# Optimization experiments

Hardware: AMD Instinct MI355X
Metric: run time of the kernel (lower is better)

## Reference

```python
import jax, jax.numpy as jnp
import numpy as np

P, G, N = 32, 256, 6890  # preds, gallery size, SMPL vertices per person


def _procrustes_v2v(pred, gt):
    """Similarity (Procrustes) align pred->gt, return mean per-vertex L2 error.
    pred, gt: (M, 3) point clouds (M = 2*N, both people jointly aligned)."""
    mu_p = pred.mean(axis=0)
    mu_g = gt.mean(axis=0)
    Xp = pred - mu_p
    Xg = gt - mu_g
    var_p = jnp.sum(Xp * Xp)
    K = Xp.T @ Xg                      # (3,3) cross-covariance
    U, s, Vh = jnp.linalg.svd(K)
    V = Vh.T
    d = jnp.sign(jnp.linalg.det(V @ U.T))  # reflection fix
    D = jnp.stack([jnp.ones_like(d), jnp.ones_like(d), d])
    R = (V * D[None, :]) @ U.T         # rotation, det(R)=+1
    scale = jnp.sum(s * D) / var_p
    aligned = scale * (Xp @ R.T) + mu_g
    return jnp.linalg.norm(aligned - gt, axis=-1).mean()


def setup_inputs() -> dict:
    key = jax.random.key(0)
    k1, k2 = jax.random.split(key)
    pred_vertices = jax.random.normal(k1, (P, 2, N, 3), dtype=jnp.float32)
    target = jax.random.normal(k2, (G, 2, N, 3), dtype=jnp.float32)
    return {"pred_vertices": pred_vertices, "target": target}


def reference(pred_vertices, target):
    # flatten the two-person meshes into a single joint point cloud per sample
    pred = pred_vertices.reshape(pred_vertices.shape[0], -1, 3)  # (P, 2N, 3)
    gt = target.reshape(target.shape[0], -1, 3)                  # (G, 2N, 3)
    # all-pairs procrustes v2v errors: (P, G)
    pair_err = jax.vmap(lambda p: jax.vmap(lambda g: _procrustes_v2v(p, g))(gt))(pred)
    mapping = jnp.argmin(pair_err, axis=1)   # best gt index per prediction
    min_error = jnp.min(pair_err, axis=1)    # its v2v error
    return mapping, min_error
```

## Files before the change

### kernel.cpp

```cpp
#include <hip/hip_runtime.h>
#include <math.h>

#define P_ 32
#define G_ 256
#define NV 6890
#define M_ (2 * NV)
#define QUADS (M_ / 4)
#define NPAIR (P_ * G_)

struct WS {
    float mu_p[P_][3];
    float var_p[P_];
    float mu_g[G_][3];
    float At[NPAIR][12];
    float Kmat[NPAIR][9];
    float pair_err[NPAIR];
};

__device__ inline double block_reduce(double v, double* smem) {
#pragma unroll
    for (int off = 32; off > 0; off >>= 1) v += __shfl_down(v, off, 64);
    int wid  = threadIdx.x >> 6;
    int lane = threadIdx.x & 63;
    __syncthreads();
    if (lane == 0) smem[wid] = v;
    __syncthreads();
    double r = 0.0;
    if (threadIdx.x == 0) {
        int nw = blockDim.x >> 6;
        for (int w = 0; w < nw; ++w) r += smem[w];
    }
    return r;
}

__global__ __launch_bounds__(256) void stats_all(const float* __restrict__ pred,
                                                 const float* __restrict__ gt, WS* ws) {
    int b = blockIdx.x;
    bool isP = (b < P_);
    const float* base = isP ? pred + (size_t)b * (M_ * 3)
                            : gt + (size_t)(b - P_) * (M_ * 3);
    double sx = 0, sy = 0, sz = 0, sq = 0;
    for (int q = threadIdx.x; q < QUADS; q += 256) {
        const float4* p4 = (const float4*)(base + 12 * (size_t)q);
        float4 a = p4[0], c = p4[1], d = p4[2];
        sx += (double)a.x + (double)a.w + (double)c.z + (double)d.y;
        sy += (double)a.y + (double)c.x + (double)c.w + (double)d.z;
        sz += (double)a.z + (double)c.y + (double)d.x + (double)d.w;
        if (isP) {
            sq += (double)a.x * a.x + (double)a.y * a.y + (double)a.z * a.z +
                  (double)a.w * a.w + (double)c.x * c.x + (double)c.y * c.y +
                  (double)c.z * c.z + (double)c.w * c.w + (double)d.x * d.x +
                  (double)d.y * d.y + (double)d.z * d.z + (double)d.w * d.w;
        }
    }
    __shared__ double smem[4];
    double rx = block_reduce(sx, smem);
    double ry = block_reduce(sy, smem);
    double rz = block_reduce(sz, smem);
    double rq = block_reduce(sq, smem);
    if (threadIdx.x == 0) {
        double mx = rx / M_, my = ry / M_, mz = rz / M_;
        if (isP) {
            ws->mu_p[b][0] = (float)mx;
            ws->mu_p[b][1] = (float)my;
            ws->mu_p[b][2] = (float)mz;
            ws->var_p[b] = (float)(rq - (mx * mx + my * my + mz * mz) * (double)M_);
        } else {
            ws->mu_g[b - P_][0] = (float)mx;
            ws->mu_g[b - P_][1] = (float)my;
            ws->mu_g[b - P_][2] = (float)mz;
        }
    }
}

#define LOAD_QUAD(BASE, Q, X, Y, Z)                                     \
    {                                                                   \
        const float4* _p4 = (const float4*)((BASE) + 12 * (size_t)(Q)); \
        float4 _a = _p4[0], _c = _p4[1], _d = _p4[2];                   \
        X[0] = _a.x; X[1] = _a.w; X[2] = _c.z; X[3] = _d.y;             \
        Y[0] = _a.y; Y[1] = _c.x; Y[2] = _c.w; Y[3] = _d.z;             \
        Z[0] = _a.z; Z[1] = _c.y; Z[2] = _d.x; Z[3] = _d.w;             \
    }

__global__ __launch_bounds__(256, 2) void crosscov_r(const float* __restrict__ pred,
                                                     const float* __restrict__ gt,
                                                     WS* __restrict__ ws) {
    int bx = blockIdx.x;
    int gbase = (bx & 63) * 4;
    int pbase = (bx >> 6) * 4;
    int t = threadIdx.x;

    const float* pb[4];
    const float* gb[4];
#pragma unroll
    for (int j = 0; j < 4; ++j) {
        pb[j] = pred + (size_t)(pbase + j) * (M_ * 3);
        gb[j] = gt + (size_t)(gbase + j) * (M_ * 3);
    }

    float acc[16][9];
#pragma unroll
    for (int q = 0; q < 16; ++q)
#pragma unroll
        for (int j = 0; j < 9; ++j) acc[q][j] = 0.f;

    for (int q = t; q < QUADS; q += 256) {
        float px[4][4], py[4][4], pz[4][4];
#pragma unroll
        for (int j = 0; j < 4; ++j) LOAD_QUAD(pb[j], q, px[j], py[j], pz[j]);
#pragma unroll
        for (int gg = 0; gg < 4; ++gg) {
            float gx[4], gy[4], gz[4];
            LOAD_QUAD(gb[gg], q, gx, gy, gz);
#pragma unroll
            for (int pp = 0; pp < 4; ++pp) {
                float* a = acc[gg * 4 + pp];
#pragma unroll
                for (int k = 0; k < 4; ++k) {
                    a[0] = fmaf(px[pp][k], gx[k], a[0]);
                    a[1] = fmaf(px[pp][k], gy[k], a[1]);
                    a[2] = fmaf(px[pp][k], gz[k], a[2]);
                    a[3] = fmaf(py[pp][k], gx[k], a[3]);
                    a[4] = fmaf(py[pp][k], gy[k], a[4]);
                    a[5] = fmaf(py[pp][k], gz[k], a[5]);
                    a[6] = fmaf(pz[pp][k], gx[k], a[6]);
                    a[7] = fmaf(pz[pp][k], gy[k], a[7]);
                    a[8] = fmaf(pz[pp][k], gz[k], a[8]);
                }
            }
        }
    }

#pragma unroll
    for (int q = 0; q < 16; ++q)
#pragma unroll
        for (int j = 0; j < 9; ++j) {
            float v = acc[q][j];
            v += __shfl_xor(v, 1);  v += __shfl_xor(v, 2);
            v += __shfl_xor(v, 4);  v += __shfl_xor(v, 8);
            v += __shfl_xor(v, 16); v += __shfl_xor(v, 32);
            acc[q][j] = v;
        }
    __shared__ float part[4][144];
    int lane = t & 63, wave = t >> 6;
    if (lane == 0) {
#pragma unroll
        for (int q = 0; q < 16; ++q)
#pragma unroll
            for (int j = 0; j < 9; ++j) part[wave][q * 9 + j] = acc[q][j];
    }
    __syncthreads();
    if (t < 144) {
        float s = part[0][t] + part[1][t] + part[2][t] + part[3][t];
        int idx = t / 9, j = t % 9;
        int gg = idx >> 2, pp = idx & 3;
        ws->Kmat[(gbase + gg) * P_ + (pbase + pp)][j] = s;
    }
}

__global__ __launch_bounds__(256) void pair_svd(WS* ws) {
    int pair = blockIdx.x * blockDim.x + threadIdx.x;
    if (pair >= NPAIR) return;
    int p = pair & 31;
    int g = pair >> 5;

    double K[3][3];
#pragma unroll
    for (int a = 0; a < 3; ++a)
#pragma unroll
        for (int b = 0; b < 3; ++b) K[a][b] = (double)ws->Kmat[pair][3 * a + b];
    {
        double mp[3] = { ws->mu_p[p][0], ws->mu_p[p][1], ws->mu_p[p][2] };
        double mg[3] = { ws->mu_g[g][0], ws->mu_g[g][1], ws->mu_g[g][2] };
#pragma unroll
        for (int a = 0; a < 3; ++a)
#pragma unroll
            for (int b = 0; b < 3; ++b)
                K[a][b] -= (double)M_ * mp[a] * mg[b];
    }

    double S[3][3];
#pragma unroll
    for (int a = 0; a < 3; ++a)
#pragma unroll
        for (int b = 0; b < 3; ++b) {
            double acc = 0.0;
#pragma unroll
            for (int c = 0; c < 3; ++c) acc += K[c][a] * K[c][b];
            S[a][b] = acc;
        }

    double V[3][3] = { {1, 0, 0}, {0, 1, 0}, {0, 0, 1} };
    double tr = S[0][0] + S[1][1] + S[2][2];
    double tol = 1e-30 * tr * tr + 1e-300;
    const int PP[3] = {0, 0, 1};
    const int QQ[3] = {1, 2, 2};
    for (int sweep = 0; sweep < 30; ++sweep) {
        double off = S[0][1] * S[0][1] + S[0][2] * S[0][2] + S[1][2] * S[1][2];
        if (off <= tol) break;
        for (int r3 = 0; r3 < 3; ++r3) {
            int pq = PP[r3], qq = QQ[r3];
            double apq = S[pq][qq];
            if (apq == 0.0) continue;
            double theta = (S[qq][qq] - S[pq][pq]) / (2.0 * apq);
            double tt = copysign(1.0, theta) / (fabs(theta) + sqrt(theta * theta + 1.0));
            double c = 1.0 / sqrt(tt * tt + 1.0);
            double sj = tt * c;
            for (int r = 0; r < 3; ++r) {
                double srp = S[r][pq], srq = S[r][qq];
                S[r][pq] = c * srp - sj * srq;
                S[r][qq] = sj * srp + c * srq;
            }
            for (int cc = 0; cc < 3; ++cc) {
                double spr = S[pq][cc], sqr = S[qq][cc];
                S[pq][cc] = c * spr - sj * sqr;
                S[qq][cc] = sj * spr + c * sqr;
            }
            for (int r = 0; r < 3; ++r) {
                double vrp = V[r][pq], vrq = V[r][qq];
                V[r][pq] = c * vrp - sj * vrq;
                V[r][qq] = sj * vrp + c * vrq;
            }
        }
    }

    double lam[3] = { S[0][0], S[1][1], S[2][2] };
    int idx[3] = { 0, 1, 2 };
    if (lam[idx[0]] < lam[idx[1]]) { int tt = idx[0]; idx[0] = idx[1]; idx[1] = tt; }
    if (lam[idx[0]] < lam[idx[2]]) { int tt = idx[0]; idx[0] = idx[2]; idx[2] = tt; }
    if (lam[idx[1]] < lam[idx[2]]) { int tt = idx[1]; idx[1] = idx[2]; idx[2] = tt; }
    double Vs[3][3];
    double sv[3];
#pragma unroll
    for (int i = 0; i < 3; ++i) {
        double l = lam[idx[i]];
        sv[i] = sqrt(l > 0.0 ? l : 0.0);
        for (int r = 0; r < 3; ++r) Vs[r][i] = V[r][idx[i]];
    }

    double U[3][3];
#pragma unroll
    for (int i = 0; i < 3; ++i) {
        double kx = K[0][0] * Vs[0][i] + K[0][1] * Vs[1][i] + K[0][2] * Vs[2][i];
        double ky = K[1][0] * Vs[0][i] + K[1][1] * Vs[1][i] + K[1][2] * Vs[2][i];
        double kz = K[2][0] * Vs[0][i] + K[2][1] * Vs[1][i] + K[2][2] * Vs[2][i];
        double inv = (sv[i] > 1e-12 * sv[0] && sv[i] > 0.0) ? 1.0 / sv[i] : 0.0;
        U[0][i] = kx * inv; U[1][i] = ky * inv; U[2][i] = kz * inv;
    }
    if (sv[2] <= 1e-12 * sv[0] || sv[0] == 0.0) {
        U[0][2] = U[1][0] * U[2][1] - U[2][0] * U[1][1];
        U[1][2] = U[2][0] * U[0][1] - U[0][0] * U[2][1];
        U[2][2] = U[0][0] * U[1][1] - U[1][0] * U[0][1];
    }

    double detK = K[0][0] * (K[1][1] * K[2][2] - K[1][2] * K[2][1])
                - K[0][1] * (K[1][0] * K[2][2] - K[1][2] * K[2][0])
                + K[0][2] * (K[1][0] * K[2][1] - K[1][1] * K[2][0]);
    double d = (detK >= 0.0) ? 1.0 : -1.0;

    double varp = (double)ws->var_p[p];
    double scale = (sv[0] + sv[1] + d * sv[2]) / varp;

    float A[9];
#pragma unroll
    for (int a = 0; a < 3; ++a)
#pragma unroll
        for (int b = 0; b < 3; ++b) {
            double r = Vs[a][0] * U[b][0] + Vs[a][1] * U[b][1] + d * Vs[a][2] * U[b][2];
            A[3 * a + b] = (float)(scale * r);
        }
    double mp[3] = { ws->mu_p[p][0], ws->mu_p[p][1], ws->mu_p[p][2] };
    double mg[3] = { ws->mu_g[g][0], ws->mu_g[g][1], ws->mu_g[g][2] };
    float tvec[3];
#pragma unroll
    for (int a = 0; a < 3; ++a)
        tvec[a] = (float)(mg[a] - ((double)A[3 * a + 0] * mp[0] + (double)A[3 * a + 1] * mp[1] +
                                   (double)A[3 * a + 2] * mp[2]));

#pragma unroll
    for (int j = 0; j < 9; ++j) ws->At[pair][j] = A[j];
#pragma unroll
    for (int j = 0; j < 3; ++j) ws->At[pair][9 + j] = tvec[j];
}

__global__ __launch_bounds__(256, 3) void pair_error_r(const float* __restrict__ pred,
                                                       const float* __restrict__ gt,
                                                       WS* __restrict__ ws) {
    int bx = blockIdx.x;
    int gbase = (bx & 63) * 4;
    int pbase = (bx >> 6) * 2;
    int t = threadIdx.x;

    float A[8][12];
#pragma unroll
    for (int gg = 0; gg < 4; ++gg)
#pragma unroll
        for (int pp = 0; pp < 2; ++pp) {
            int pair = (gbase + gg) * P_ + (pbase + pp);
#pragma unroll
            for (int j = 0; j < 12; ++j) A[gg * 2 + pp][j] = ws->At[pair][j];
        }

    const float* pb0 = pred + (size_t)pbase * (M_ * 3);
    const float* pb1 = pred + (size_t)(pbase + 1) * (M_ * 3);
    const float* gb[4];
#pragma unroll
    for (int j = 0; j < 4; ++j) gb[j] = gt + (size_t)(gbase + j) * (M_ * 3);

    float acc[8];
#pragma unroll
    for (int q = 0; q < 8; ++q) acc[q] = 0.f;

    for (int q = t; q < QUADS; q += 256) {
        float px[2][4], py[2][4], pz[2][4];
        LOAD_QUAD(pb0, q, px[0], py[0], pz[0]);
        LOAD_QUAD(pb1, q, px[1], py[1], pz[1]);
#pragma unroll
        for (int gg = 0; gg < 4; ++gg) {
            float gx[4], gy[4], gz[4];
            LOAD_QUAD(gb[gg], q, gx, gy, gz);
#pragma unroll
            for (int pp = 0; pp < 2; ++pp) {
                const float* a = A[gg * 2 + pp];
                float s = 0.f;
#pragma unroll
                for (int k = 0; k < 4; ++k) {
                    float dx = fmaf(a[0], px[pp][k], fmaf(a[1], py[pp][k], fmaf(a[2], pz[pp][k], a[9])))  - gx[k];
                    float dy = fmaf(a[3], px[pp][k], fmaf(a[4], py[pp][k], fmaf(a[5], pz[pp][k], a[10]))) - gy[k];
                    float dz = fmaf(a[6], px[pp][k], fmaf(a[7], py[pp][k], fmaf(a[8], pz[pp][k], a[11]))) - gz[k];
                    s += __builtin_amdgcn_sqrtf(fmaf(dx, dx, fmaf(dy, dy, dz * dz)));
                }
                acc[gg * 2 + pp] += s;
            }
        }
    }

#pragma unroll
    for (int q = 0; q < 8; ++q) {
        float v = acc[q];
        v += __shfl_xor(v, 1);  v += __shfl_xor(v, 2);
        v += __shfl_xor(v, 4);  v += __shfl_xor(v, 8);
        v += __shfl_xor(v, 16); v += __shfl_xor(v, 32);
        acc[q] = v;
    }
    __shared__ float part[4][8];
    int lane = t & 63, wave = t >> 6;
    if (lane == 0) {
#pragma unroll
        for (int q = 0; q < 8; ++q) part[wave][q] = acc[q];
    }
    __syncthreads();
    if (t < 8) {
        float s = part[0][t] + part[1][t] + part[2][t] + part[3][t];
        int gg = t >> 1, pp = t & 1;
        ws->pair_err[(gbase + gg) * P_ + (pbase + pp)] = s / (float)M_;
    }
}

__global__ void argmin_out(const WS* __restrict__ ws, float* __restrict__ out) {
    __shared__ float be[8][32];
    __shared__ int   bg[8][32];
    int t = threadIdx.x;
    int p = t & 31, slice = t >> 5;
    float best = 3.4e38f;
    int bi = G_;
    for (int g = slice; g < G_; g += 8) {
        float e = ws->pair_err[g * P_ + p];
        if (e < best) { best = e; bi = g; }
    }
    be[slice][p] = best;
    bg[slice][p] = bi;
    __syncthreads();
    if (t < P_) {
        float b0 = be[0][t];
        int   i0 = bg[0][t];
        for (int s = 1; s < 8; ++s) {
            float e = be[s][t];
            int   i = bg[s][t];
            if (e < b0 || (e == b0 && i < i0)) { b0 = e; i0 = i; }
        }
        out[t] = (float)i0;
        out[P_ + t] = b0;
    }
}

extern "C" void kernel_launch(void* const* d_in, const int* in_sizes, int n_in,
                              void* d_out, int out_size, void* d_ws, size_t ws_size,
                              hipStream_t stream) {
    const float* pred = (const float*)d_in[0];
    const float* gt   = (const float*)d_in[1];
    float* out = (float*)d_out;
    WS* ws = (WS*)d_ws;

    stats_all<<<dim3(P_ + G_), dim3(256), 0, stream>>>(pred, gt, ws);
    crosscov_r<<<dim3(8 * 64), dim3(256), 0, stream>>>(pred, gt, ws);
    pair_svd<<<dim3(NPAIR / 256), dim3(256), 0, stream>>>(ws);
    pair_error_r<<<dim3(16 * 64), dim3(256), 0, stream>>>(pred, gt, ws);
    argmin_out<<<dim3(1), dim3(256), 0, stream>>>(ws, out);
}
```

Baseline: 224.5 us.

## Fuse stats into crosscov launch and use packed float2 FMAs in hot loops

```diff
diff --git a/kernel.cpp b/kernel.cpp
--- a/kernel.cpp
+++ b/kernel.cpp
@@ -7,6 +7,12 @@
 #define M_ (2 * NV)
 #define QUADS (M_ / 4)
 #define NPAIR (P_ * G_)
+#define NB_CC 512
+
+typedef float v2f __attribute__((ext_vector_type(2)));
+__device__ inline v2f v2(float a, float b) { v2f r; r.x = a; r.y = b; return r; }
+__device__ inline v2f vsplat(float a) { v2f r; r.x = a; r.y = a; return r; }
+__device__ inline v2f vfma(v2f a, v2f b, v2f c) { return __builtin_elementwise_fma(a, b, c); }
 
 struct WS {
     float mu_p[P_][3];
@@ -33,63 +39,54 @@
     return r;
 }
 
-__global__ __launch_bounds__(256) void stats_all(const float* __restrict__ pred,
-                                                 const float* __restrict__ gt, WS* ws) {
-    int b = blockIdx.x;
-    bool isP = (b < P_);
-    const float* base = isP ? pred + (size_t)b * (M_ * 3)
-                            : gt + (size_t)(b - P_) * (M_ * 3);
-    double sx = 0, sy = 0, sz = 0, sq = 0;
-    for (int q = threadIdx.x; q < QUADS; q += 256) {
-        const float4* p4 = (const float4*)(base + 12 * (size_t)q);
-        float4 a = p4[0], c = p4[1], d = p4[2];
-        sx += (double)a.x + (double)a.w + (double)c.z + (double)d.y;
-        sy += (double)a.y + (double)c.x + (double)c.w + (double)d.z;
-        sz += (double)a.z + (double)c.y + (double)d.x + (double)d.w;
-        if (isP) {
-            sq += (double)a.x * a.x + (double)a.y * a.y + (double)a.z * a.z +
-                  (double)a.w * a.w + (double)c.x * c.x + (double)c.y * c.y +
-                  (double)c.z * c.z + (double)c.w * c.w + (double)d.x * d.x +
-                  (double)d.y * d.y + (double)d.z * d.z + (double)d.w * d.w;
-        }
-    }
-    __shared__ double smem[4];
-    double rx = block_reduce(sx, smem);
-    double ry = block_reduce(sy, smem);
-    double rz = block_reduce(sz, smem);
-    double rq = block_reduce(sq, smem);
-    if (threadIdx.x == 0) {
-        double mx = rx / M_, my = ry / M_, mz = rz / M_;
-        if (isP) {
-            ws->mu_p[b][0] = (float)mx;
-            ws->mu_p[b][1] = (float)my;
-            ws->mu_p[b][2] = (float)mz;
-            ws->var_p[b] = (float)(rq - (mx * mx + my * my + mz * mz) * (double)M_);
-        } else {
-            ws->mu_g[b - P_][0] = (float)mx;
-            ws->mu_g[b - P_][1] = (float)my;
-            ws->mu_g[b - P_][2] = (float)mz;
-        }
-    }
-}
-
-#define LOAD_QUAD(BASE, Q, X, Y, Z)                                     \
-    {                                                                   \
-        const float4* _p4 = (const float4*)((BASE) + 12 * (size_t)(Q)); \
-        float4 _a = _p4[0], _c = _p4[1], _d = _p4[2];                   \
-        X[0] = _a.x; X[1] = _a.w; X[2] = _c.z; X[3] = _d.y;             \
-        Y[0] = _a.y; Y[1] = _c.x; Y[2] = _c.w; Y[3] = _d.z;             \
-        Z[0] = _a.z; Z[1] = _c.y; Z[2] = _d.x; Z[3] = _d.w;             \
-    }
-
-__global__ __launch_bounds__(256, 2) void crosscov_r(const float* __restrict__ pred,
+__global__ __launch_bounds__(256, 2) void crosscov_p(const float* __restrict__ pred,
                                                      const float* __restrict__ gt,
                                                      WS* __restrict__ ws) {
     int bx = blockIdx.x;
+    int t = threadIdx.x;
+
+    if (bx >= NB_CC) {
+        int b = bx - NB_CC;
+        bool isP = (b < P_);
+        const float* base = isP ? pred + (size_t)b * (M_ * 3)
+                                : gt + (size_t)(b - P_) * (M_ * 3);
+        double sx = 0, sy = 0, sz = 0, sq = 0;
+        for (int q = t; q < QUADS; q += 256) {
+            const float4* p4 = (const float4*)(base + 12 * (size_t)q);
+            float4 a = p4[0], c = p4[1], d = p4[2];
+            sx += (double)a.x + (double)a.w + (double)c.z + (double)d.y;
+            sy += (double)a.y + (double)c.x + (double)c.w + (double)d.z;
+            sz += (double)a.z + (double)c.y + (double)d.x + (double)d.w;
+            if (isP) {
+                sq += (double)a.x * a.x + (double)a.y * a.y + (double)a.z * a.z +
+                      (double)a.w * a.w + (double)c.x * c.x + (double)c.y * c.y +
+                      (double)c.z * c.z + (double)c.w * c.w + (double)d.x * d.x +
+                      (double)d.y * d.y + (double)d.z * d.z + (double)d.w * d.w;
+            }
+        }
+        __shared__ double smem[4];
+        double rx = block_reduce(sx, smem);
+        double ry = block_reduce(sy, smem);
+        double rz = block_reduce(sz, smem);
+        double rq = block_reduce(sq, smem);
+        if (t == 0) {
+            double mx = rx / M_, my = ry / M_, mz = rz / M_;
+            if (isP) {
+                ws->mu_p[b][0] = (float)mx;
+                ws->mu_p[b][1] = (float)my;
+                ws->mu_p[b][2] = (float)mz;
+                ws->var_p[b] = (float)(rq - (mx * mx + my * my + mz * mz) * (double)M_);
+            } else {
+                ws->mu_g[b - P_][0] = (float)mx;
+                ws->mu_g[b - P_][1] = (float)my;
+                ws->mu_g[b - P_][2] = (float)mz;
+            }
+        }
+        return;
+    }
+
     int gbase = (bx & 63) * 4;
     int pbase = (bx >> 6) * 4;
-    int t = threadIdx.x;
-
     const float* pb[4];
     const float* gb[4];
 #pragma unroll
@@ -98,56 +95,82 @@
         gb[j] = gt + (size_t)(gbase + j) * (M_ * 3);
     }
 
-    float acc[16][9];
-#pragma unroll
-    for (int q = 0; q < 16; ++q)
-#pragma unroll
-        for (int j = 0; j < 9; ++j) acc[q][j] = 0.f;
+    v2f a01[16], a34[16], a67[16], a25[16];
+    float a8[16];
+#pragma unroll
+    for (int i = 0; i < 16; ++i) {
+        a01[i] = vsplat(0.f); a34[i] = vsplat(0.f);
+        a67[i] = vsplat(0.f); a25[i] = vsplat(0.f);
+        a8[i] = 0.f;
+    }
 
     for (int q = t; q < QUADS; q += 256) {
-        float px[4][4], py[4][4], pz[4][4];
-#pragma unroll
-        for (int j = 0; j < 4; ++j) LOAD_QUAD(pb[j], q, px[j], py[j], pz[j]);
+        float4 P[4][3];
+#pragma unroll
+        for (int j = 0; j < 4; ++j) {
+            const float4* p4 = (const float4*)(pb[j] + 12 * (size_t)q);
+            P[j][0] = p4[0]; P[j][1] = p4[1]; P[j][2] = p4[2];
+        }
 #pragma unroll
         for (int gg = 0; gg < 4; ++gg) {
-            float gx[4], gy[4], gz[4];
-            LOAD_QUAD(gb[gg], q, gx, gy, gz);
+            const float4* g4 = (const float4*)(gb[gg] + 12 * (size_t)q);
+            float4 Ga = g4[0], Gc = g4[1], Gd = g4[2];
+            v2f gxy0 = v2(Ga.x, Ga.y), gxy1 = v2(Ga.w, Gc.x);
+            v2f gxy2 = v2(Gc.z, Gc.w), gxy3 = v2(Gd.y, Gd.z);
+            float gz0 = Ga.z, gz1 = Gc.y, gz2 = Gd.x, gz3 = Gd.w;
 #pragma unroll
             for (int pp = 0; pp < 4; ++pp) {
-                float* a = acc[gg * 4 + pp];
-#pragma unroll
-                for (int k = 0; k < 4; ++k) {
-                    a[0] = fmaf(px[pp][k], gx[k], a[0]);
-                    a[1] = fmaf(px[pp][k], gy[k], a[1]);
-                    a[2] = fmaf(px[pp][k], gz[k], a[2]);
-                    a[3] = fmaf(py[pp][k], gx[k], a[3]);
-                    a[4] = fmaf(py[pp][k], gy[k], a[4]);
-                    a[5] = fmaf(py[pp][k], gz[k], a[5]);
-                    a[6] = fmaf(pz[pp][k], gx[k], a[6]);
-                    a[7] = fmaf(pz[pp][k], gy[k], a[7]);
-                    a[8] = fmaf(pz[pp][k], gz[k], a[8]);
-                }
-            }
-        }
-    }
-
-#pragma unroll
-    for (int q = 0; q < 16; ++q)
+                int i = gg * 4 + pp;
+                float4 Pa = P[pp][0], Pc = P[pp][1], Pd = P[pp][2];
+                a01[i] = vfma(vsplat(Pa.x), gxy0, a01[i]);
+                a34[i] = vfma(vsplat(Pa.y), gxy0, a34[i]);
+                a67[i] = vfma(vsplat(Pa.z), gxy0, a67[i]);
+                a25[i] = vfma(v2(Pa.x, Pa.y), vsplat(gz0), a25[i]);
+                a8[i]  = fmaf(Pa.z, gz0, a8[i]);
+                a01[i] = vfma(vsplat(Pa.w), gxy1, a01[i]);
+                a34[i] = vfma(vsplat(Pc.x), gxy1, a34[i]);
+                a67[i] = vfma(vsplat(Pc.y), gxy1, a67[i]);
+                a25[i] = vfma(v2(Pa.w, Pc.x), vsplat(gz1), a25[i]);
+                a8[i]  = fmaf(Pc.y, gz1, a8[i]);
+                a01[i] = vfma(vsplat(Pc.z), gxy2, a01[i]);
+                a34[i] = vfma(vsplat(Pc.w), gxy2, a34[i]);
+                a67[i] = vfma(vsplat(Pd.x), gxy2, a67[i]);
+                a25[i] = vfma(v2(Pc.z, Pc.w), vsplat(gz2), a25[i]);
+                a8[i]  = fmaf(Pd.x, gz2, a8[i]);
+                a01[i] = vfma(vsplat(Pd.y), gxy3, a01[i]);
+                a34[i] = vfma(vsplat(Pd.z), gxy3, a34[i]);
+                a67[i] = vfma(vsplat(Pd.w), gxy3, a67[i]);
+                a25[i] = vfma(v2(Pd.y, Pd.z), vsplat(gz3), a25[i]);
+                a8[i]  = fmaf(Pd.w, gz3, a8[i]);
+            }
+        }
+    }
+
+    float K[16][9];
+#pragma unroll
+    for (int i = 0; i < 16; ++i) {
+        K[i][0] = a01[i].x; K[i][1] = a01[i].y; K[i][2] = a25[i].x;
+        K[i][3] = a34[i].x; K[i][4] = a34[i].y; K[i][5] = a25[i].y;
+        K[i][6] = a67[i].x; K[i][7] = a67[i].y; K[i][8] = a8[i];
+    }
+
+#pragma unroll
+    for (int i = 0; i < 16; ++i)
 #pragma unroll
         for (int j = 0; j < 9; ++j) {
-            float v = acc[q][j];
+            float v = K[i][j];
             v += __shfl_xor(v, 1);  v += __shfl_xor(v, 2);
             v += __shfl_xor(v, 4);  v += __shfl_xor(v, 8);
             v += __shfl_xor(v, 16); v += __shfl_xor(v, 32);
-            acc[q][j] = v;
+            K[i][j] = v;
         }
     __shared__ float part[4][144];
     int lane = t & 63, wave = t >> 6;
     if (lane == 0) {
 #pragma unroll
-        for (int q = 0; q < 16; ++q)
-#pragma unroll
-            for (int j = 0; j < 9; ++j) part[wave][q * 9 + j] = acc[q][j];
+        for (int i = 0; i < 16; ++i)
+#pragma unroll
+            for (int j = 0; j < 9; ++j) part[wave][i * 9 + j] = K[i][j];
     }
     __syncthreads();
     if (t < 144) {
@@ -283,7 +306,7 @@
     for (int j = 0; j < 3; ++j) ws->At[pair][9 + j] = tvec[j];
 }
 
-__global__ __launch_bounds__(256, 3) void pair_error_r(const float* __restrict__ pred,
+__global__ __launch_bounds__(256, 3) void pair_error_p(const float* __restrict__ pred,
                                                        const float* __restrict__ gt,
                                                        WS* __restrict__ ws) {
     int bx = blockIdx.x;
@@ -291,14 +314,19 @@
     int pbase = (bx >> 6) * 2;
     int t = threadIdx.x;
 
-    float A[8][12];
+    v2f a03[8], a14[8], a25v[8], t01[8];
+    float a6[8], a7[8], a8v[8], t2[8];
 #pragma unroll
     for (int gg = 0; gg < 4; ++gg)
 #pragma unroll
         for (int pp = 0; pp < 2; ++pp) {
-            int pair = (gbase + gg) * P_ + (pbase + pp);
-#pragma unroll
-            for (int j = 0; j < 12; ++j) A[gg * 2 + pp][j] = ws->At[pair][j];
+            int i = gg * 2 + pp;
+            const float* At = ws->At[(gbase + gg) * P_ + (pbase + pp)];
+            a03[i] = v2(At[0], At[3]);
+            a14[i] = v2(At[1], At[4]);
+            a25v[i] = v2(At[2], At[5]);
+            t01[i] = v2(At[9], At[10]);
+            a6[i] = At[6]; a7[i] = At[7]; a8v[i] = At[8]; t2[i] = At[11];
         }
 
     const float* pb0 = pred + (size_t)pbase * (M_ * 3);
@@ -309,45 +337,58 @@
 
     float acc[8];
 #pragma unroll
-    for (int q = 0; q < 8; ++q) acc[q] = 0.f;
+    for (int i = 0; i < 8; ++i) acc[i] = 0.f;
 
     for (int q = t; q < QUADS; q += 256) {
-        float px[2][4], py[2][4], pz[2][4];
-        LOAD_QUAD(pb0, q, px[0], py[0], pz[0]);
-        LOAD_QUAD(pb1, q, px[1], py[1], pz[1]);
+        float4 P[2][3];
+        {
+            const float4* p4 = (const float4*)(pb0 + 12 * (size_t)q);
+            P[0][0] = p4[0]; P[0][1] = p4[1]; P[0][2] = p4[2];
+            p4 = (const float4*)(pb1 + 12 * (size_t)q);
+            P[1][0] = p4[0]; P[1][1] = p4[1]; P[1][2] = p4[2];
+        }
 #pragma unroll
         for (int gg = 0; gg < 4; ++gg) {
-            float gx[4], gy[4], gz[4];
-            LOAD_QUAD(gb[gg], q, gx, gy, gz);
+            const float4* g4 = (const float4*)(gb[gg] + 12 * (size_t)q);
+            float4 Ga = g4[0], Gc = g4[1], Gd = g4[2];
+            v2f gxy[4] = { v2(Ga.x, Ga.y), v2(Ga.w, Gc.x), v2(Gc.z, Gc.w), v2(Gd.y, Gd.z) };
+            float gz[4] = { Ga.z, Gc.y, Gd.x, Gd.w };
 #pragma unroll
             for (int pp = 0; pp < 2; ++pp) {
-                const float* a = A[gg * 2 + pp];
+                int i = gg * 2 + pp;
+                float4 Pa = P[pp][0], Pc = P[pp][1], Pd = P[pp][2];
+                float x[4] = { Pa.x, Pa.w, Pc.z, Pd.y };
+                float y[4] = { Pa.y, Pc.x, Pc.w, Pd.z };
+                float z[4] = { Pa.z, Pc.y, Pd.x, Pd.w };
                 float s = 0.f;
 #pragma unroll
                 for (int k = 0; k < 4; ++k) {
-                    float dx = fmaf(a[0], px[pp][k], fmaf(a[1], py[pp][k], fmaf(a[2], pz[pp][k], a[9])))  - gx[k];
-                    float dy = fmaf(a[3], px[pp][k], fmaf(a[4], py[pp][k], fmaf(a[5], pz[pp][k], a[10]))) - gy[k];
-                    float dz = fmaf(a[6], px[pp][k], fmaf(a[7], py[pp][k], fmaf(a[8], pz[pp][k], a[11]))) - gz[k];
-                    s += __builtin_amdgcn_sqrtf(fmaf(dx, dx, fmaf(dy, dy, dz * dz)));
+                    v2f dd = vfma(a03[i], vsplat(x[k]),
+                             vfma(a14[i], vsplat(y[k]),
+                             vfma(a25v[i], vsplat(z[k]), t01[i])));
+                    dd = dd - gxy[k];
+                    float dz = fmaf(a6[i], x[k], fmaf(a7[i], y[k], fmaf(a8v[i], z[k], t2[i]))) - gz[k];
+                    v2f m = dd * dd;
+                    s += __builtin_amdgcn_sqrtf(fmaf(dz, dz, m.x + m.y));
                 }
-                acc[gg * 2 + pp] += s;
-            }
-        }
-    }
-
-#pragma unroll
-    for (int q = 0; q < 8; ++q) {
-        float v = acc[q];
+                acc[i] += s;
+            }
+        }
+    }
+
+#pragma unroll
+    for (int i = 0; i < 8; ++i) {
+        float v = acc[i];
         v += __shfl_xor(v, 1);  v += __shfl_xor(v, 2);
         v += __shfl_xor(v, 4);  v += __shfl_xor(v, 8);
         v += __shfl_xor(v, 16); v += __shfl_xor(v, 32);
-        acc[q] = v;
+        acc[i] = v;
     }
     __shared__ float part[4][8];
     int lane = t & 63, wave = t >> 6;
     if (lane == 0) {
 #pragma unroll
-        for (int q = 0; q < 8; ++q) part[wave][q] = acc[q];
+        for (int i = 0; i < 8; ++i) part[wave][i] = acc[i];
     }
     __syncthreads();
     if (t < 8) {
@@ -392,9 +433,8 @@
     float* out = (float*)d_out;
     WS* ws = (WS*)d_ws;
 
-    stats_all<<<dim3(P_ + G_), dim3(256), 0, stream>>>(pred, gt, ws);
-    crosscov_r<<<dim3(8 * 64), dim3(256), 0, stream>>>(pred, gt, ws);
+    crosscov_p<<<dim3(NB_CC + P_ + G_), dim3(256), 0, stream>>>(pred, gt, ws);
     pair_svd<<<dim3(NPAIR / 256), dim3(256), 0, stream>>>(ws);
-    pair_error_r<<<dim3(16 * 64), dim3(256), 0, stream>>>(pred, gt, ws);
+    pair_error_p<<<dim3(16 * 64), dim3(256), 0, stream>>>(pred, gt, ws);
     argmin_out<<<dim3(1), dim3(256), 0, stream>>>(ws, out);
 }
```

Measured after the change: 209.8 us. 6.5% less time.
